# Optimization experiments

Hardware: AMD Instinct MI355X
Metric: run time of the kernel (lower is better)

The kernel has to match this reference:

```python
import jax, jax.numpy as jnp
import numpy as np


def setup_inputs() -> dict:
    key = jax.random.key(0)
    ks = jax.random.split(key, 10)
    B, T = 1024, 8192
    # X features: [time, current I, temperature T, voltage U]
    t = jnp.cumsum(jax.random.uniform(ks[0], (B, T, 1), jnp.float32) + 0.5, axis=1)  # increasing time
    feats = jax.random.normal(ks[1], (B, T, 3), jnp.float32)
    X = jnp.concatenate([t, feats], axis=-1)  # [B, T, 4]
    # SC: [Q (capacity), eta_0, R, SOC_init_base]; keep Q away from 0
    SC = jax.random.uniform(ks[2], (B, 4), jnp.float32, minval=0.5, maxval=1.5)
    std = 0.1
    # SOC_init_net: Linear(4,1) -> Softplus -> Linear(1,1), normal(0,0.1) weights, zero bias
    W1i = jax.random.normal(ks[3], (1, 4), jnp.float32) * std
    b1i = jnp.zeros((1,), jnp.float32)
    W2i = jax.random.normal(ks[4], (1, 1), jnp.float32) * std
    b2i = jnp.zeros((1,), jnp.float32)
    # eta_net: Linear(2,1) -> Softplus -> Linear(1,1)
    W1e = jax.random.normal(ks[5], (1, 2), jnp.float32) * std
    b1e = jnp.zeros((1,), jnp.float32)
    W2e = jax.random.normal(ks[6], (1, 1), jnp.float32) * std
    b2e = jnp.zeros((1,), jnp.float32)
    return {"X": X, "SC": SC, "W1i": W1i, "b1i": b1i, "W2i": W2i, "b2i": b2i,
            "W1e": W1e, "b1e": b1e, "W2e": W2e, "b2e": b2e}


def reference(X, SC, W1i, b1i, W2i, b2i, W1e, b1e, W2e, b2e):
    # X: [B, T, 4] = (t, I, Temp, U); SC: [B, 4] = (Q, eta_0, R, soc_base)
    I = X[..., 1:2]      # [B, T, 1]
    Temp = X[..., 2:3]   # [B, T, 1]
    U = X[..., 3:4]      # [B, T, 1]
    R = SC[..., 2:3]     # [B, 1]
    # SOC_init_net on first-timestep features
    feat0 = jnp.concatenate([I[:, 0, :], Temp[:, 0, :], U[:, 0, :], R], axis=-1)  # [B, 4]
    h0 = jax.nn.softplus(feat0 @ W1i.T + b1i)
    soc_net = h0 @ W2i.T + b2i                     # [B, 1]
    SOC_init = SC[..., 3:4] * (1.0 + soc_net)      # [B, 1]
    # eta_net over all timesteps
    feat = jnp.concatenate([I, Temp], axis=-1)     # [B, T, 2]
    h = jax.nn.softplus(feat @ W1e.T + b1e)
    delta_eta = h @ W2e.T + b2e                    # [B, T, 1]
    # ODE RHS: dSOC/dt = eta_0 * (1 + delta_eta) * I / (3600 * Q)
    Q = SC[..., 0:1][:, None, :]                   # [B, 1, 1]
    eta0 = SC[..., 1:2][:, None, :]                # [B, 1, 1]
    f = eta0 * (1.0 + delta_eta) * I / (3600.0 * Q)  # [B, T, 1]
    # Euler integration: y_{k+1} = y_k + (t_{k+1} - t_k) * f(x_k, y_k); f independent of y -> cumsum
    ts = X[..., 0:1]                               # [B, T, 1]
    dt = ts[:, 1:] - ts[:, :-1]                    # [B, T-1, 1]
    incr = dt * f[:, :-1]                          # [B, T-1, 1]
    zero = jnp.zeros_like(SOC_init)[:, None, :]    # [B, 1, 1]
    SOC = SOC_init[:, None, :] + jnp.concatenate([zero, jnp.cumsum(incr, axis=1)], axis=1)
    return SOC                                     # [B, T, 1]
```

## Files before the change

### kernel.cpp

```cpp
#include <hip/hip_runtime.h>
#include <type_traits>


static __device__ __forceinline__ float bf2f(unsigned int u) {
    union { unsigned int i; float f; } v;
    v.i = u << 16;
    return v.f;
}
static __device__ __forceinline__ unsigned short f2bf(float f) {
    union { unsigned int i; float f; } v;
    v.f = f;
    unsigned int x = v.i;
    return (unsigned short)((x + 0x7fffu + ((x >> 16) & 1u)) >> 16);
}
static __device__ __forceinline__ float sp_fast(float x) {
    return __logf(1.f + __expf(x));
}

struct F4 { float ts, I, Te, U; };
static __device__ __forceinline__ F4 dec(ushort4 x) {
    return {bf2f(x.x), bf2f(x.y), bf2f(x.z), bf2f(x.w)};
}
static __device__ __forceinline__ F4 dec(float4 x) {
    return {x.x, x.y, x.z, x.w};
}

template <bool BF16>
static __device__ __forceinline__ float ld(const void* p, int i) {
    return BF16 ? bf2f(((const unsigned short*)p)[i]) : ((const float*)p)[i];
}

constexpr int BLOCK = 256;

template <int NCH>
static __device__ void scan_k4(
    const float* __restrict__ X, const float* __restrict__ SC,
    const float* __restrict__ W1i, const float* __restrict__ b1i,
    const float* __restrict__ W2i, const float* __restrict__ b2i,
    const float* __restrict__ W1e, const float* __restrict__ b1e,
    const float* __restrict__ W2e, const float* __restrict__ b2e,
    float* __restrict__ outv, float* s_wtot, float* s_init)
{
    constexpr int SPAN = NCH * 256;
    constexpr int T    = SPAN * 4;

    const int b    = blockIdx.x;
    const int tid  = threadIdx.x;
    const int lane = tid & 63;
    const int wave = tid >> 6;
    const int ws   = wave * SPAN;

    const float Q    = SC[b * 4 + 0];
    const float eta0 = SC[b * 4 + 1];
    const float R    = SC[b * 4 + 2];
    const float S3   = SC[b * 4 + 3];
    const float w1e0 = W1e[0];
    const float w1e1 = W1e[1];
    const float vb1e = b1e[0];
    const float coef = eta0 / (3600.f * Q);
    const float c2   = coef * W2e[0];
    const float c1   = coef * (1.f + b2e[0]);

    const float4* Xrow = (const float4*)X + (size_t)b * T;

    float4 ring[8];
    #pragma unroll
    for (int c = 0; c < 2; ++c)
        #pragma unroll
        for (int j = 0; j < 4; ++j)
            ring[c * 4 + j] = Xrow[ws + c * 256 + lane * 4 + j];

    float ts_c, f_c;
    if (wave > 0) {
        const float4 vp = Xrow[ws - 1];
        const float hp = sp_fast(fmaf(vp.y, w1e0, fmaf(vp.z, w1e1, vb1e)));
        f_c  = fmaf(c2, hp, c1) * vp.y;
        ts_c = vp.x;
    } else {
        const float4 v0 = Xrow[0];
        ts_c = v0.x;
        f_c  = 0.f;
        const float pre = fmaf(v0.y, W1i[0],
                          fmaf(v0.z, W1i[1],
                          fmaf(v0.w, W1i[2],
                          fmaf(R, W1i[3], b1i[0]))));
        const float h0 = sp_fast(pre);
        if (lane == 0)
            *s_init = S3 * (1.f + fmaf(h0, W2i[0], b2i[0]));
    }

    float vals[NCH * 4];
    float carry = 0.f;
    #pragma unroll
    for (int c = 0; c < NCH; ++c) {
        const int s = (c & 1) * 4;
        const float4 v0 = ring[s + 0];
        const float4 v1 = ring[s + 1];
        const float4 v2 = ring[s + 2];
        const float4 v3 = ring[s + 3];
        if (c + 2 < NCH) {
            #pragma unroll
            for (int j = 0; j < 4; ++j)
                ring[s + j] = Xrow[ws + (c + 2) * 256 + lane * 4 + j];
        }

        const float f0 = fmaf(c2, sp_fast(fmaf(v0.y, w1e0, fmaf(v0.z, w1e1, vb1e))), c1) * v0.y;
        const float f1 = fmaf(c2, sp_fast(fmaf(v1.y, w1e0, fmaf(v1.z, w1e1, vb1e))), c1) * v1.y;
        const float f2 = fmaf(c2, sp_fast(fmaf(v2.y, w1e0, fmaf(v2.z, w1e1, vb1e))), c1) * v2.y;
        const float f3 = fmaf(c2, sp_fast(fmaf(v3.y, w1e0, fmaf(v3.z, w1e1, vb1e))), c1) * v3.y;

        float pts = __shfl_up(v3.x, 1, 64);
        float pf  = __shfl_up(f3,   1, 64);
        if (lane == 0) { pts = ts_c; pf = f_c; }

        const float g0 = (v0.x - pts) * pf;
        const float g1 = fmaf(v1.x - v0.x, f0, g0);
        const float g2 = fmaf(v2.x - v1.x, f1, g1);
        const float g3 = fmaf(v3.x - v2.x, f2, g2);

        float S = g3;
        #pragma unroll
        for (int d = 1; d < 64; d <<= 1) {
            const float u = __shfl_up(S, d, 64);
            if (lane >= d) S += u;
        }
        const float tb = carry + (S - g3);
        vals[c * 4 + 0] = g0 + tb;
        vals[c * 4 + 1] = g1 + tb;
        vals[c * 4 + 2] = g2 + tb;
        vals[c * 4 + 3] = g3 + tb;

        carry += __shfl(S, 63, 64);
        ts_c   = __shfl(v3.x, 63, 64);
        f_c    = __shfl(f3, 63, 64);
    }
    if (lane == 0) s_wtot[wave] = carry;
    __syncthreads();

    float base = *s_init;
    #pragma unroll
    for (int w = 0; w < 3; ++w)
        if (w < wave) base += s_wtot[w];

    float4* orow = (float4*)(outv + (size_t)b * T);
    #pragma unroll
    for (int c = 0; c < NCH; ++c) {
        float4 o;
        o.x = vals[c * 4 + 0] + base;
        o.y = vals[c * 4 + 1] + base;
        o.z = vals[c * 4 + 2] + base;
        o.w = vals[c * 4 + 3] + base;
        orow[wave * (SPAN / 4) + c * 64 + lane] = o;
    }
}

__global__ __launch_bounds__(BLOCK, 4) void socnet_reg(
    const void* __restrict__ X, const void* __restrict__ SC,
    const void* __restrict__ W1i, const void* __restrict__ b1i,
    const void* __restrict__ W2i, const void* __restrict__ b2i,
    const void* __restrict__ W1e, const void* __restrict__ b1e,
    const void* __restrict__ W2e, const void* __restrict__ b2e,
    void* __restrict__ out)
{
    __shared__ float s_wtot[4];
    __shared__ float s_init;
    scan_k4<8>((const float*)X, (const float*)SC,
               (const float*)W1i, (const float*)b1i,
               (const float*)W2i, (const float*)b2i,
               (const float*)W1e, (const float*)b1e,
               (const float*)W2e, (const float*)b2e,
               (float*)out, s_wtot, &s_init);
}

template <bool BF16>
static __device__ void scan_serial(
    const void* __restrict__ Xv, const void* __restrict__ SCv,
    const void* __restrict__ W1i, const void* __restrict__ b1i,
    const void* __restrict__ W2i, const void* __restrict__ b2i,
    const void* __restrict__ W1e, const void* __restrict__ b1e,
    const void* __restrict__ W2e, const void* __restrict__ b2e,
    void* __restrict__ outv, int T,
    float* s_wts, float* s_wf, float* s_wsum, float* s_carr)
{
    using XVec = typename std::conditional<BF16, ushort4, float4>::type;
    const int b = blockIdx.x, tid = threadIdx.x;
    const int lane = tid & 63, wave = tid >> 6;
    const int ntile = (T + BLOCK - 1) / BLOCK;

    const float Q    = ld<BF16>(SCv, b * 4 + 0);
    const float eta0 = ld<BF16>(SCv, b * 4 + 1);
    const float R    = ld<BF16>(SCv, b * 4 + 2);
    const float S3   = ld<BF16>(SCv, b * 4 + 3);
    const float w1e0 = ld<BF16>(W1e, 0);
    const float w1e1 = ld<BF16>(W1e, 1);
    const float vb1e = ld<BF16>(b1e, 0);
    const float coef = eta0 / (3600.f * Q);
    const float c2   = coef * ld<BF16>(W2e, 0);
    const float c1   = coef * (1.f + ld<BF16>(b2e, 0));

    const XVec* Xrow = (const XVec*)Xv + (size_t)b * T;

    for (int tile = 0; tile < ntile; ++tile) {
        const int t = tile * BLOCK + tid;
        const bool act = t < T;
        F4 v = {0.f, 0.f, 0.f, 0.f};
        if (act) v = dec(Xrow[t]);
        const float f = fmaf(c2, sp_fast(fmaf(v.I, w1e0, fmaf(v.Te, w1e1, vb1e))), c1) * v.I;

        float pts = __shfl_up(v.ts, 1, 64);
        float pf  = __shfl_up(f, 1, 64);

        __syncthreads();
        if (lane == 63) { s_wts[wave] = v.ts; s_wf[wave] = f; }
        if (tile == 0 && tid == 0) {
            const float pre = fmaf(v.I, ld<BF16>(W1i, 0),
                              fmaf(v.Te, ld<BF16>(W1i, 1),
                              fmaf(v.U, ld<BF16>(W1i, 2),
                              fmaf(R, ld<BF16>(W1i, 3), ld<BF16>(b1i, 0)))));
            s_carr[0] = S3 * (1.f + fmaf(sp_fast(pre), ld<BF16>(W2i, 0), ld<BF16>(b2i, 0)));
        }
        __syncthreads();
        if (lane == 0) {
            if (wave == 0) { if (tile > 0) { pts = s_carr[1]; pf = s_carr[2]; } }
            else { pts = s_wts[wave - 1]; pf = s_wf[wave - 1]; }
        }
        float g = (t == 0 || !act) ? 0.f : (v.ts - pts) * pf;
        #pragma unroll
        for (int d = 1; d < 64; d <<= 1) {
            const float u = __shfl_up(g, d, 64);
            if (lane >= d) g += u;
        }
        if (lane == 63) s_wsum[wave] = g;
        __syncthreads();
        float soc = s_carr[0];
        #pragma unroll
        for (int w = 0; w < 3; ++w) if (w < wave) soc += s_wsum[w];
        soc += g;
        if (act) {
            if (BF16) ((unsigned short*)outv)[(size_t)b * T + t] = f2bf(soc);
            else      ((float*)outv)[(size_t)b * T + t] = soc;
        }
        __syncthreads();
        if (tid == BLOCK - 1) { s_carr[0] = soc; s_carr[1] = v.ts; s_carr[2] = f; }
    }
}

__global__ __launch_bounds__(BLOCK) void socnet_serial_k(
    const void* __restrict__ X, const void* __restrict__ SC,
    const void* __restrict__ W1i, const void* __restrict__ b1i,
    const void* __restrict__ W2i, const void* __restrict__ b2i,
    const void* __restrict__ W1e, const void* __restrict__ b1e,
    const void* __restrict__ W2e, const void* __restrict__ b2e,
    void* __restrict__ out, int T)
{
    __shared__ float s_wts[4], s_wf[4], s_wsum[4], s_carr[3];
    const unsigned int* scw = (const unsigned int*)SC;
    const float l0 = bf2f(scw[0] & 0xFFFFu), l1 = bf2f(scw[1] & 0xFFFFu);
    const float l2 = bf2f(scw[2] & 0xFFFFu), l3 = bf2f(scw[3] & 0xFFFFu);
    const bool isbf =
        (l0 >= 0.45f && l0 <= 1.55f) && (l1 >= 0.45f && l1 <= 1.55f) &&
        (l2 >= 0.45f && l2 <= 1.55f) && (l3 >= 0.45f && l3 <= 1.55f);
    if (isbf) scan_serial<true >(X, SC, W1i, b1i, W2i, b2i, W1e, b1e, W2e, b2e,
                                 out, T, s_wts, s_wf, s_wsum, s_carr);
    else      scan_serial<false>(X, SC, W1i, b1i, W2i, b2i, W1e, b1e, W2e, b2e,
                                 out, T, s_wts, s_wf, s_wsum, s_carr);
}

extern "C" void kernel_launch(void* const* d_in, const int* in_sizes, int n_in,
                              void* d_out, int out_size, void* d_ws, size_t ws_size,
                              hipStream_t stream) {
    const int B = in_sizes[1] / 4;
    const int T = in_sizes[0] / (B * 4);

    if (T == 8192) {
        socnet_reg<<<dim3(B), dim3(BLOCK), 0, stream>>>(
            d_in[0], d_in[1], d_in[2], d_in[3], d_in[4], d_in[5],
            d_in[6], d_in[7], d_in[8], d_in[9], d_out);
    } else {
        socnet_serial_k<<<dim3(B), dim3(BLOCK), 0, stream>>>(
            d_in[0], d_in[1], d_in[2], d_in[3], d_in[4], d_in[5],
            d_in[6], d_in[7], d_in[8], d_in[9], d_out, T);
    }
}
```

Before: 215.0 us.

## Rotate per-block chunk processing order to spread memory channel access

Each block now starts its per-wave scan at a rotated chunk offset chosen from the block index. The scan is split into two runs that are stitched back together with an extra carry correction. The aim is to stop many blocks from hitting the same address ranges or memory channels at the same moment. The cost is an extra boundary load, runtime-dependent chunk indexing and slightly more register pressure.

```diff
diff --git a/kernel.cpp b/kernel.cpp
--- a/kernel.cpp
+++ b/kernel.cpp
@@ -33,13 +33,13 @@
 constexpr int BLOCK = 256;
 
 template <int NCH>
-static __device__ void scan_k4(
+static __device__ void scan_rot(
     const float* __restrict__ X, const float* __restrict__ SC,
     const float* __restrict__ W1i, const float* __restrict__ b1i,
     const float* __restrict__ W2i, const float* __restrict__ b2i,
     const float* __restrict__ W1e, const float* __restrict__ b1e,
     const float* __restrict__ W2e, const float* __restrict__ b2e,
-    float* __restrict__ outv, float* s_wtot, float* s_init)
+    float* __restrict__ outv, int R, float* s_wtot, float* s_init)
 {
     constexpr int SPAN = NCH * 256;
     constexpr int T    = SPAN * 4;
@@ -52,7 +52,7 @@
 
     const float Q    = SC[b * 4 + 0];
     const float eta0 = SC[b * 4 + 1];
-    const float R    = SC[b * 4 + 2];
+    const float Rsc  = SC[b * 4 + 2];
     const float S3   = SC[b * 4 + 3];
     const float w1e0 = W1e[0];
     const float w1e1 = W1e[1];
@@ -65,58 +65,72 @@
 
     float4 ring[8];
     #pragma unroll
-    for (int c = 0; c < 2; ++c)
+    for (int c = 0; c < 2; ++c) {
+        const int ch = (c + R) & (NCH - 1);
         #pragma unroll
         for (int j = 0; j < 4; ++j)
-            ring[c * 4 + j] = Xrow[ws + c * 256 + lane * 4 + j];
-
+            ring[c * 4 + j] = Xrow[ws + ch * 256 + lane * 4 + j];
+    }
+
+    float4 p1v = {0.f, 0.f, 0.f, 0.f};
+    if (R > 0) p1v = Xrow[ws + R * 256 - 1];
+    const float4 p2v = (wave > 0) ? Xrow[ws - 1] : Xrow[0];
+
+    float ts2, f2;
+    if (wave > 0) {
+        const float hp = sp_fast(fmaf(p2v.y, w1e0, fmaf(p2v.z, w1e1, vb1e)));
+        f2  = fmaf(c2, hp, c1) * p2v.y;
+        ts2 = p2v.x;
+    } else {
+        ts2 = p2v.x;
+        f2  = 0.f;
+    }
     float ts_c, f_c;
-    if (wave > 0) {
-        const float4 vp = Xrow[ws - 1];
-        const float hp = sp_fast(fmaf(vp.y, w1e0, fmaf(vp.z, w1e1, vb1e)));
-        f_c  = fmaf(c2, hp, c1) * vp.y;
-        ts_c = vp.x;
+    if (R > 0) {
+        const float hp = sp_fast(fmaf(p1v.y, w1e0, fmaf(p1v.z, w1e1, vb1e)));
+        f_c  = fmaf(c2, hp, c1) * p1v.y;
+        ts_c = p1v.x;
     } else {
-        const float4 v0 = Xrow[0];
-        ts_c = v0.x;
-        f_c  = 0.f;
-        const float pre = fmaf(v0.y, W1i[0],
-                          fmaf(v0.z, W1i[1],
-                          fmaf(v0.w, W1i[2],
-                          fmaf(R, W1i[3], b1i[0]))));
-        const float h0 = sp_fast(pre);
-        if (lane == 0)
-            *s_init = S3 * (1.f + fmaf(h0, W2i[0], b2i[0]));
+        ts_c = ts2;
+        f_c  = f2;
     }
 
     float vals[NCH * 4];
     float carry = 0.f;
+    float run1_total = 0.f;
     #pragma unroll
-    for (int c = 0; c < NCH; ++c) {
-        const int s = (c & 1) * 4;
+    for (int ci = 0; ci < NCH; ++ci) {
+        if (R > 0 && ci == NCH - R) {
+            run1_total = carry;
+            carry = 0.f;
+            ts_c = ts2;
+            f_c  = f2;
+        }
+        const int s = (ci & 1) * 4;
         const float4 v0 = ring[s + 0];
         const float4 v1 = ring[s + 1];
         const float4 v2 = ring[s + 2];
         const float4 v3 = ring[s + 3];
-        if (c + 2 < NCH) {
+        if (ci + 2 < NCH) {
+            const int chn = (ci + 2 + R) & (NCH - 1);
             #pragma unroll
             for (int j = 0; j < 4; ++j)
-                ring[s + j] = Xrow[ws + (c + 2) * 256 + lane * 4 + j];
-        }
-
-        const float f0 = fmaf(c2, sp_fast(fmaf(v0.y, w1e0, fmaf(v0.z, w1e1, vb1e))), c1) * v0.y;
-        const float f1 = fmaf(c2, sp_fast(fmaf(v1.y, w1e0, fmaf(v1.z, w1e1, vb1e))), c1) * v1.y;
-        const float f2 = fmaf(c2, sp_fast(fmaf(v2.y, w1e0, fmaf(v2.z, w1e1, vb1e))), c1) * v2.y;
-        const float f3 = fmaf(c2, sp_fast(fmaf(v3.y, w1e0, fmaf(v3.z, w1e1, vb1e))), c1) * v3.y;
+                ring[s + j] = Xrow[ws + chn * 256 + lane * 4 + j];
+        }
+
+        const float f0  = fmaf(c2, sp_fast(fmaf(v0.y, w1e0, fmaf(v0.z, w1e1, vb1e))), c1) * v0.y;
+        const float f1  = fmaf(c2, sp_fast(fmaf(v1.y, w1e0, fmaf(v1.z, w1e1, vb1e))), c1) * v1.y;
+        const float fv2 = fmaf(c2, sp_fast(fmaf(v2.y, w1e0, fmaf(v2.z, w1e1, vb1e))), c1) * v2.y;
+        const float f3  = fmaf(c2, sp_fast(fmaf(v3.y, w1e0, fmaf(v3.z, w1e1, vb1e))), c1) * v3.y;
 
         float pts = __shfl_up(v3.x, 1, 64);
         float pf  = __shfl_up(f3,   1, 64);
         if (lane == 0) { pts = ts_c; pf = f_c; }
 
         const float g0 = (v0.x - pts) * pf;
-        const float g1 = fmaf(v1.x - v0.x, f0, g0);
-        const float g2 = fmaf(v2.x - v1.x, f1, g1);
-        const float g3 = fmaf(v3.x - v2.x, f2, g2);
+        const float g1 = fmaf(v1.x - v0.x, f0,  g0);
+        const float g2 = fmaf(v2.x - v1.x, f1,  g1);
+        const float g3 = fmaf(v3.x - v2.x, fv2, g2);
 
         float S = g3;
         #pragma unroll
@@ -125,16 +139,28 @@
             if (lane >= d) S += u;
         }
         const float tb = carry + (S - g3);
-        vals[c * 4 + 0] = g0 + tb;
-        vals[c * 4 + 1] = g1 + tb;
-        vals[c * 4 + 2] = g2 + tb;
-        vals[c * 4 + 3] = g3 + tb;
+        vals[ci * 4 + 0] = g0 + tb;
+        vals[ci * 4 + 1] = g1 + tb;
+        vals[ci * 4 + 2] = g2 + tb;
+        vals[ci * 4 + 3] = g3 + tb;
 
         carry += __shfl(S, 63, 64);
         ts_c   = __shfl(v3.x, 63, 64);
         f_c    = __shfl(f3, 63, 64);
     }
-    if (lane == 0) s_wtot[wave] = carry;
+    float run2_total, wave_total;
+    if (R > 0) { run2_total = carry; wave_total = run1_total + run2_total; }
+    else       { run2_total = 0.f;   wave_total = carry; }
+
+    if (wave == 0 && lane == 0) {
+        const float pre = fmaf(p2v.y, W1i[0],
+                          fmaf(p2v.z, W1i[1],
+                          fmaf(p2v.w, W1i[2],
+                          fmaf(Rsc, W1i[3], b1i[0]))));
+        const float h0 = sp_fast(pre);
+        *s_init = S3 * (1.f + fmaf(h0, W2i[0], b2i[0]));
+    }
+    if (lane == 0) s_wtot[wave] = wave_total;
     __syncthreads();
 
     float base = *s_init;
@@ -144,13 +170,15 @@
 
     float4* orow = (float4*)(outv + (size_t)b * T);
     #pragma unroll
-    for (int c = 0; c < NCH; ++c) {
+    for (int ci = 0; ci < NCH; ++ci) {
+        const int ch = (ci + R) & (NCH - 1);
+        const float badd = base + ((ci < NCH - R) ? run2_total : 0.f);
         float4 o;
-        o.x = vals[c * 4 + 0] + base;
-        o.y = vals[c * 4 + 1] + base;
-        o.z = vals[c * 4 + 2] + base;
-        o.w = vals[c * 4 + 3] + base;
-        orow[wave * (SPAN / 4) + c * 64 + lane] = o;
+        o.x = vals[ci * 4 + 0] + badd;
+        o.y = vals[ci * 4 + 1] + badd;
+        o.z = vals[ci * 4 + 2] + badd;
+        o.w = vals[ci * 4 + 3] + badd;
+        orow[wave * (SPAN / 4) + ch * 64 + lane] = o;
     }
 }
 
@@ -164,12 +192,13 @@
 {
     __shared__ float s_wtot[4];
     __shared__ float s_init;
-    scan_k4<8>((const float*)X, (const float*)SC,
-               (const float*)W1i, (const float*)b1i,
-               (const float*)W2i, (const float*)b2i,
-               (const float*)W1e, (const float*)b1e,
-               (const float*)W2e, (const float*)b2e,
-               (float*)out, s_wtot, &s_init);
+    const int r = (blockIdx.x >> 3) & 7;
+    scan_rot<8>((const float*)X, (const float*)SC,
+                (const float*)W1i, (const float*)b1i,
+                (const float*)W2i, (const float*)b2i,
+                (const float*)W1e, (const float*)b1e,
+                (const float*)W2e, (const float*)b2e,
+                (float*)out, r, s_wtot, &s_init);
 }
 
 template <bool BF16>
```

After: 229.7 us. +6.8%, slower.

## Split per-row scan into reduce-then-scan kernels over eight segments

Applied to the files above, without the earlier changes.

Replaces the one-block-per-row scan with two kernels. The first computes per-segment totals for eight 1024-step segments of each row, plus SOC_init, into workspace. The second recomputes f, adds the carried prefix of earlier segments, and writes the outputs. This gives eight times more blocks to fill the GPU, at the cost of reading X twice and an extra launch. Any bf16 input path is dropped for the T=8192 case.

```diff
diff --git a/kernel.cpp b/kernel.cpp
--- a/kernel.cpp
+++ b/kernel.cpp
@@ -31,6 +31,186 @@
 }
 
 constexpr int BLOCK = 256;
+
+__global__ __launch_bounds__(BLOCK, 6) void socnet_tot(
+    const void* __restrict__ Xv, const void* __restrict__ SCv,
+    const void* __restrict__ W1iv, const void* __restrict__ b1iv,
+    const void* __restrict__ W2iv, const void* __restrict__ b2iv,
+    const void* __restrict__ W1ev, const void* __restrict__ b1ev,
+    const void* __restrict__ W2ev, const void* __restrict__ b2ev,
+    float* __restrict__ ws, int B)
+{
+    const float* X   = (const float*)Xv;
+    const float* SC  = (const float*)SCv;
+    const float* W1i = (const float*)W1iv;
+    const float* b1i = (const float*)b1iv;
+    const float* W2i = (const float*)W2iv;
+    const float* b2i = (const float*)b2iv;
+    const float* W1e = (const float*)W1ev;
+    const float* b1e = (const float*)b1ev;
+    const float* W2e = (const float*)W2ev;
+    const float* b2e = (const float*)b2ev;
+
+    const int blk  = blockIdx.x;
+    const int b    = blk >> 3;
+    const int s    = blk & 7;
+    const int tid  = threadIdx.x;
+    const int lane = tid & 63;
+    const int wave = tid >> 6;
+
+    const float Q    = SC[b * 4 + 0];
+    const float eta0 = SC[b * 4 + 1];
+    const float Rsc  = SC[b * 4 + 2];
+    const float S3   = SC[b * 4 + 3];
+    const float w1e0 = W1e[0];
+    const float w1e1 = W1e[1];
+    const float vb1e = b1e[0];
+    const float coef = eta0 / (3600.f * Q);
+    const float c2   = coef * W2e[0];
+    const float c1   = coef * (1.f + b2e[0]);
+
+    const float4* Xrow = (const float4*)X + (size_t)b * 8192;
+    const int base = s * 1024;
+
+    const float4 v0 = Xrow[base + tid * 4 + 0];
+    const float4 v1 = Xrow[base + tid * 4 + 1];
+    const float4 v2 = Xrow[base + tid * 4 + 2];
+    const float4 v3 = Xrow[base + tid * 4 + 3];
+
+    float4 vp; float ts_c, f_c;
+    if (s == 0 && wave == 0) {
+        vp = Xrow[0];
+        ts_c = vp.x;
+        f_c  = 0.f;
+    } else {
+        vp = Xrow[base + wave * 256 - 1];
+        ts_c = vp.x;
+        f_c  = fmaf(c2, sp_fast(fmaf(vp.y, w1e0, fmaf(vp.z, w1e1, vb1e))), c1) * vp.y;
+    }
+
+    const float f0 = fmaf(c2, sp_fast(fmaf(v0.y, w1e0, fmaf(v0.z, w1e1, vb1e))), c1) * v0.y;
+    const float f1 = fmaf(c2, sp_fast(fmaf(v1.y, w1e0, fmaf(v1.z, w1e1, vb1e))), c1) * v1.y;
+    const float f2 = fmaf(c2, sp_fast(fmaf(v2.y, w1e0, fmaf(v2.z, w1e1, vb1e))), c1) * v2.y;
+    const float f3 = fmaf(c2, sp_fast(fmaf(v3.y, w1e0, fmaf(v3.z, w1e1, vb1e))), c1) * v3.y;
+
+    float pts = __shfl_up(v3.x, 1, 64);
+    float pf  = __shfl_up(f3,   1, 64);
+    if (lane == 0) { pts = ts_c; pf = f_c; }
+
+    float gsum = (v0.x - pts) * pf;
+    gsum = fmaf(v1.x - v0.x, f0, gsum);
+    gsum = fmaf(v2.x - v1.x, f1, gsum);
+    gsum = fmaf(v3.x - v2.x, f2, gsum);
+
+    #pragma unroll
+    for (int d = 1; d < 64; d <<= 1)
+        gsum += __shfl_xor(gsum, d, 64);
+
+    __shared__ float sred[4];
+    if (lane == 0) sred[wave] = gsum;
+    __syncthreads();
+    if (tid == 0)
+        ws[b * 8 + s] = sred[0] + sred[1] + sred[2] + sred[3];
+
+    if (s == 0 && tid == 0) {
+        const float pre = fmaf(vp.y, W1i[0],
+                          fmaf(vp.z, W1i[1],
+                          fmaf(vp.w, W1i[2],
+                          fmaf(Rsc, W1i[3], b1i[0]))));
+        ws[B * 8 + b] = S3 * (1.f + fmaf(sp_fast(pre), W2i[0], b2i[0]));
+    }
+}
+
+__global__ __launch_bounds__(BLOCK, 6) void socnet_scan(
+    const void* __restrict__ Xv, const void* __restrict__ SCv,
+    const void* __restrict__ W1ev, const void* __restrict__ b1ev,
+    const void* __restrict__ W2ev, const void* __restrict__ b2ev,
+    const float* __restrict__ ws, void* __restrict__ outv, int B)
+{
+    const float* X   = (const float*)Xv;
+    const float* SC  = (const float*)SCv;
+    const float* W1e = (const float*)W1ev;
+    const float* b1e = (const float*)b1ev;
+    const float* W2e = (const float*)W2ev;
+    const float* b2e = (const float*)b2ev;
+
+    const int blk  = blockIdx.x;
+    const int b    = blk >> 3;
+    const int s    = blk & 7;
+    const int tid  = threadIdx.x;
+    const int lane = tid & 63;
+    const int wave = tid >> 6;
+
+    const float Q    = SC[b * 4 + 0];
+    const float eta0 = SC[b * 4 + 1];
+    const float w1e0 = W1e[0];
+    const float w1e1 = W1e[1];
+    const float vb1e = b1e[0];
+    const float coef = eta0 / (3600.f * Q);
+    const float c2   = coef * W2e[0];
+    const float c1   = coef * (1.f + b2e[0]);
+
+    float bacc = ws[B * 8 + b];
+    #pragma unroll
+    for (int j = 0; j < 7; ++j)
+        if (j < s) bacc += ws[b * 8 + j];
+
+    const float4* Xrow = (const float4*)X + (size_t)b * 8192;
+    const int base = s * 1024;
+
+    const float4 v0 = Xrow[base + tid * 4 + 0];
+    const float4 v1 = Xrow[base + tid * 4 + 1];
+    const float4 v2 = Xrow[base + tid * 4 + 2];
+    const float4 v3 = Xrow[base + tid * 4 + 3];
+
+    float4 vp; float ts_c, f_c;
+    if (s == 0 && wave == 0) {
+        vp = Xrow[0];
+        ts_c = vp.x;
+        f_c  = 0.f;
+    } else {
+        vp = Xrow[base + wave * 256 - 1];
+        ts_c = vp.x;
+        f_c  = fmaf(c2, sp_fast(fmaf(vp.y, w1e0, fmaf(vp.z, w1e1, vb1e))), c1) * vp.y;
+    }
+
+    const float f0 = fmaf(c2, sp_fast(fmaf(v0.y, w1e0, fmaf(v0.z, w1e1, vb1e))), c1) * v0.y;
+    const float f1 = fmaf(c2, sp_fast(fmaf(v1.y, w1e0, fmaf(v1.z, w1e1, vb1e))), c1) * v1.y;
+    const float f2 = fmaf(c2, sp_fast(fmaf(v2.y, w1e0, fmaf(v2.z, w1e1, vb1e))), c1) * v2.y;
+    const float f3 = fmaf(c2, sp_fast(fmaf(v3.y, w1e0, fmaf(v3.z, w1e1, vb1e))), c1) * v3.y;
+
+    float pts = __shfl_up(v3.x, 1, 64);
+    float pf  = __shfl_up(f3,   1, 64);
+    if (lane == 0) { pts = ts_c; pf = f_c; }
+
+    const float g0 = (v0.x - pts) * pf;
+    const float g1 = fmaf(v1.x - v0.x, f0, g0);
+    const float g2 = fmaf(v2.x - v1.x, f1, g1);
+    const float g3 = fmaf(v3.x - v2.x, f2, g2);
+
+    float S = g3;
+    #pragma unroll
+    for (int d = 1; d < 64; d <<= 1) {
+        const float u = __shfl_up(S, d, 64);
+        if (lane >= d) S += u;
+    }
+
+    __shared__ float swt[4];
+    if (lane == 63) swt[wave] = S;
+    __syncthreads();
+
+    float add = bacc + (S - g3);
+    #pragma unroll
+    for (int w = 0; w < 3; ++w)
+        if (w < wave) add += swt[w];
+
+    float4 o;
+    o.x = g0 + add;
+    o.y = g1 + add;
+    o.z = g2 + add;
+    o.w = g3 + add;
+    ((float4*)outv)[(size_t)b * 2048 + s * 256 + tid] = o;
+}
 
 template <int NCH>
 static __device__ void scan_k4(
@@ -272,7 +452,17 @@
     const int B = in_sizes[1] / 4;
     const int T = in_sizes[0] / (B * 4);
 
-    if (T == 8192) {
+    const size_t ws_need = (size_t)(B * 9) * sizeof(float);
+
+    if (T == 8192 && ws_size >= ws_need && d_ws != nullptr) {
+        socnet_tot<<<dim3(B * 8), dim3(BLOCK), 0, stream>>>(
+            d_in[0], d_in[1], d_in[2], d_in[3], d_in[4], d_in[5],
+            d_in[6], d_in[7], d_in[8], d_in[9], (float*)d_ws, B);
+        socnet_scan<<<dim3(B * 8), dim3(BLOCK), 0, stream>>>(
+            d_in[0], d_in[1],
+            d_in[6], d_in[7], d_in[8], d_in[9],
+            (const float*)d_ws, d_out, B);
+    } else if (T == 8192) {
         socnet_reg<<<dim3(B), dim3(BLOCK), 0, stream>>>(
             d_in[0], d_in[1], d_in[2], d_in[3], d_in[4], d_in[5],
             d_in[6], d_in[7], d_in[8], d_in[9], d_out);
```

New measurement: 231.7 us. +7.7%, slower.

## Split each row scan across eight blocks with a two-pass carry fixup

Applied to the files above, without the earlier changes.

Replaces the one-block-per-batch-row scan with a two-kernel decomposition. The first kernel uses eight blocks per row, each computing local prefix sums of its 1024-step segment and writing segment totals and the initial SOC to workspace. The second kernel adds each segment's carry-in to the output. This aims to raise occupancy and memory parallelism over the 1024-block launch, at the cost of re-reading and re-writing the output and adding a second kernel launch.

```diff
diff --git a/kernel.cpp b/kernel.cpp
--- a/kernel.cpp
+++ b/kernel.cpp
@@ -31,6 +31,135 @@
 }
 
 constexpr int BLOCK = 256;
+
+__global__ __launch_bounds__(BLOCK, 6) void socnet_p1(
+    const void* __restrict__ Xv, const void* __restrict__ SCv,
+    const void* __restrict__ W1iv, const void* __restrict__ b1iv,
+    const void* __restrict__ W2iv, const void* __restrict__ b2iv,
+    const void* __restrict__ W1ev, const void* __restrict__ b1ev,
+    const void* __restrict__ W2ev, const void* __restrict__ b2ev,
+    float* __restrict__ ws, void* __restrict__ outv, int B)
+{
+    const float* X   = (const float*)Xv;
+    const float* SC  = (const float*)SCv;
+    const float* W1i = (const float*)W1iv;
+    const float* b1i = (const float*)b1iv;
+    const float* W2i = (const float*)W2iv;
+    const float* b2i = (const float*)b2iv;
+    const float* W1e = (const float*)W1ev;
+    const float* b1e = (const float*)b1ev;
+    const float* W2e = (const float*)W2ev;
+    const float* b2e = (const float*)b2ev;
+
+    const int blk  = blockIdx.x;
+    const int b    = blk >> 3;
+    const int s    = blk & 7;
+    const int tid  = threadIdx.x;
+    const int lane = tid & 63;
+    const int wave = tid >> 6;
+
+    const float Q    = SC[b * 4 + 0];
+    const float eta0 = SC[b * 4 + 1];
+    const float w1e0 = W1e[0];
+    const float w1e1 = W1e[1];
+    const float vb1e = b1e[0];
+    const float coef = eta0 / (3600.f * Q);
+    const float c2   = coef * W2e[0];
+    const float c1   = coef * (1.f + b2e[0]);
+
+    const float4* Xrow = (const float4*)X + (size_t)b * 8192;
+    const int seg = s * 1024;
+
+    float4 v[4];
+    #pragma unroll
+    for (int j = 0; j < 4; ++j)
+        v[j] = Xrow[seg + j * 256 + tid];
+
+    float ptsc[4], pfc[4];
+    #pragma unroll
+    for (int j = 0; j < 4; ++j) {
+        const int t0 = seg + j * 256 + wave * 64;
+        if (t0 == 0) {
+            ptsc[j] = v[j].x;
+            pfc[j]  = 0.f;
+        } else {
+            const float4 vp = Xrow[t0 - 1];
+            ptsc[j] = vp.x;
+            pfc[j]  = fmaf(c2, sp_fast(fmaf(vp.y, w1e0, fmaf(vp.z, w1e1, vb1e))), c1) * vp.y;
+        }
+    }
+
+    float Sv[4];
+    #pragma unroll
+    for (int j = 0; j < 4; ++j) {
+        const float fj = fmaf(c2, sp_fast(fmaf(v[j].y, w1e0, fmaf(v[j].z, w1e1, vb1e))), c1) * v[j].y;
+        float pts = __shfl_up(v[j].x, 1, 64);
+        float pf  = __shfl_up(fj,     1, 64);
+        if (lane == 0) { pts = ptsc[j]; pf = pfc[j]; }
+        float S = (v[j].x - pts) * pf;
+        #pragma unroll
+        for (int d = 1; d < 64; d <<= 1) {
+            const float u = __shfl_up(S, d, 64);
+            if (lane >= d) S += u;
+        }
+        Sv[j] = S;
+    }
+
+    __shared__ float s_wt[4][4];
+    #pragma unroll
+    for (int j = 0; j < 4; ++j)
+        if (lane == 63) s_wt[j][wave] = Sv[j];
+    __syncthreads();
+
+    float ctot[4];
+    #pragma unroll
+    for (int j = 0; j < 4; ++j)
+        ctot[j] = s_wt[j][0] + s_wt[j][1] + s_wt[j][2] + s_wt[j][3];
+
+    float* orow = (float*)outv + (size_t)b * 8192;
+    float cb = 0.f;
+    #pragma unroll
+    for (int j = 0; j < 4; ++j) {
+        float add = cb;
+        #pragma unroll
+        for (int w = 0; w < 3; ++w)
+            if (w < wave) add += s_wt[j][w];
+        orow[seg + j * 256 + tid] = Sv[j] + add;
+        cb += ctot[j];
+    }
+
+    if (tid == 0) {
+        ws[blk] = ctot[0] + ctot[1] + ctot[2] + ctot[3];
+        if (s == 0) {
+            const float4 x0 = Xrow[0];
+            const float pre = fmaf(x0.y, W1i[0],
+                              fmaf(x0.z, W1i[1],
+                              fmaf(x0.w, W1i[2],
+                              fmaf(SC[b * 4 + 2], W1i[3], b1i[0]))));
+            ws[B * 8 + b] = SC[b * 4 + 3] *
+                            (1.f + fmaf(sp_fast(pre), W2i[0], b2i[0]));
+        }
+    }
+}
+
+__global__ __launch_bounds__(BLOCK, 8) void socnet_p2(
+    const float* __restrict__ ws, void* __restrict__ outv, int B)
+{
+    const int blk = blockIdx.x;
+    const int b   = blk >> 3;
+    const int s   = blk & 7;
+
+    float base = ws[B * 8 + b];
+    #pragma unroll
+    for (int j = 0; j < 7; ++j)
+        if (j < s) base += ws[b * 8 + j];
+
+    float4* o4 = (float4*)outv;
+    const size_t idx = (size_t)blk * 256 + threadIdx.x;
+    float4 v = o4[idx];
+    v.x += base; v.y += base; v.z += base; v.w += base;
+    o4[idx] = v;
+}
 
 template <int NCH>
 static __device__ void scan_k4(
@@ -272,7 +401,16 @@
     const int B = in_sizes[1] / 4;
     const int T = in_sizes[0] / (B * 4);
 
-    if (T == 8192) {
+    const size_t ws_need = (size_t)(B * 9) * sizeof(float);
+
+    if (T == 8192 && ws_size >= ws_need && d_ws != nullptr) {
+        socnet_p1<<<dim3(B * 8), dim3(BLOCK), 0, stream>>>(
+            d_in[0], d_in[1], d_in[2], d_in[3], d_in[4], d_in[5],
+            d_in[6], d_in[7], d_in[8], d_in[9],
+            (float*)d_ws, d_out, B);
+        socnet_p2<<<dim3(B * 8), dim3(BLOCK), 0, stream>>>(
+            (const float*)d_ws, d_out, B);
+    } else if (T == 8192) {
         socnet_reg<<<dim3(B), dim3(BLOCK), 0, stream>>>(
             d_in[0], d_in[1], d_in[2], d_in[3], d_in[4], d_in[5],
             d_in[6], d_in[7], d_in[8], d_in[9], d_out);
```

New measurement: 224.6 us. 4.5% more time.
